# Optimization experiments

Hardware: AMD Instinct MI355X
Metric: run time of the kernel (lower is better)

The kernel has to match this reference:

```python
import jax, jax.numpy as jnp
import numpy as np

EMBED_DIM = 1024
HEAD_SIZE = 64
B, T = 8, 2048


def setup_inputs() -> dict:
    key = jax.random.key(0)
    kx, kk, kq, kv = jax.random.split(key, 4)
    s = EMBED_DIM ** -0.5  # linear init scale (arbitrary for baseline)
    return {
        "x": jax.random.normal(kx, (B, T, EMBED_DIM), dtype=jnp.float32),
        "Wk": jax.random.normal(kk, (EMBED_DIM, HEAD_SIZE), dtype=jnp.float32) * s,
        "Wq": jax.random.normal(kq, (EMBED_DIM, HEAD_SIZE), dtype=jnp.float32) * s,
        "Wv": jax.random.normal(kv, (EMBED_DIM, HEAD_SIZE), dtype=jnp.float32) * s,
    }


def reference(x, Wk, Wq, Wv):
    # x: [B, T, C]; projections: [C, H]
    k = jnp.einsum("btc,ch->bth", x, Wk)
    q = jnp.einsum("btc,ch->bth", x, Wq)
    v = jnp.einsum("btc,ch->bth", x, Wv)
    Tlen = x.shape[1]
    scores = jnp.einsum("bqh,bkh->bqk", q, k) * (Wk.shape[1] ** -0.5)  # [B,T,T]
    causal = jnp.tril(jnp.ones((Tlen, Tlen), dtype=bool))
    scores = jnp.where(causal, scores, -jnp.inf)
    weights = jax.nn.softmax(scores, axis=-1)  # dropout=0 (eval mode)
    return jnp.einsum("bqk,bkh->bqh", weights, v)
```

## Files before the change

### kernel.cpp

```cpp
#include <hip/hip_runtime.h>
#include <hip/hip_bf16.h>


typedef __attribute__((ext_vector_type(8))) __bf16 bf16x8;
typedef __attribute__((ext_vector_type(4))) float f32x4;

#define BT   16384
#define TLEN 2048
#define NB   8

__device__ __forceinline__ ushort f2bf(float f) {
    unsigned u = __builtin_bit_cast(unsigned, f);
    unsigned r = (u + 0x7FFFu + ((u >> 16) & 1u)) >> 16;
    return (ushort)r;
}

__global__ void wtrans_kernel(const float* __restrict__ Wk, const float* __restrict__ Wq,
                              const float* __restrict__ Wv, ushort* __restrict__ wtb) {
    int n = blockIdx.x;
    const float* W = (n < 64) ? Wk : (n < 128) ? Wq : Wv;
    float sc = (n >= 64 && n < 128) ? 0.125f : 1.0f;
    int h = n & 63;
    for (int k = threadIdx.x; k < 1024; k += 256)
        wtb[n * 1024 + k] = f2bf(W[(size_t)k * 64 + h] * sc);
}

__global__ __launch_bounds__(512, 3) void qkv_kernel2(
    const float* __restrict__ x, const ushort* __restrict__ wtb, ushort* __restrict__ kqv)
{
    __shared__ __align__(16) float ls_red[4][12][64][4];

    const int tid  = threadIdx.x;
    const int lane = tid & 63;
    const int wv   = tid >> 6;
    const int r    = wv & 1;
    const int h    = wv >> 1;
    const int m    = lane & 15;
    const int g    = lane >> 4;
    const int R0   = blockIdx.x * 32;
    const int arow = R0 + r * 16 + m;

    f32x4 acc[12];
    #pragma unroll
    for (int nt = 0; nt < 12; ++nt) acc[nt] = (f32x4){0.f, 0.f, 0.f, 0.f};

    const float*  xp = &x[(size_t)arow * 1024 + h * 256 + g * 8];
    const ushort* wb = &wtb[h * 256 + g * 8 + (size_t)m * 1024];

    #pragma unroll
    for (int st = 0; st < 8; ++st) {
        float4 a0 = *reinterpret_cast<const float4*>(xp);
        float4 a1 = *reinterpret_cast<const float4*>(xp + 4);
        xp += 32;
        union { ushort u[8]; bf16x8 v; } av;
        av.u[0] = f2bf(a0.x); av.u[1] = f2bf(a0.y); av.u[2] = f2bf(a0.z); av.u[3] = f2bf(a0.w);
        av.u[4] = f2bf(a1.x); av.u[5] = f2bf(a1.y); av.u[6] = f2bf(a1.z); av.u[7] = f2bf(a1.w);
        #pragma unroll
        for (int nt = 0; nt < 12; ++nt) {
            bf16x8 b = *reinterpret_cast<const bf16x8*>(wb + (size_t)nt * 16 * 1024 + st * 32);
            acc[nt] = __builtin_amdgcn_mfma_f32_16x16x32_bf16(av.v, b, acc[nt], 0, 0, 0);
        }
    }

    if (h & 1) {
        int slot = (h >> 1) * 2 + r;
        #pragma unroll
        for (int nt = 0; nt < 12; ++nt)
            *reinterpret_cast<f32x4*>(&ls_red[slot][nt][lane][0]) = acc[nt];
    }
    __syncthreads();
    if (!(h & 1)) {
        int slot = h + r;
        #pragma unroll
        for (int nt = 0; nt < 12; ++nt)
            acc[nt] += *reinterpret_cast<const f32x4*>(&ls_red[slot][nt][lane][0]);
    }
    __syncthreads();
    if (h == 2) {
        #pragma unroll
        for (int nt = 0; nt < 12; ++nt)
            *reinterpret_cast<f32x4*>(&ls_red[r][nt][lane][0]) = acc[nt];
    }
    __syncthreads();
    if (h == 0) {
        #pragma unroll
        for (int nt = 0; nt < 12; ++nt) {
            acc[nt] += *reinterpret_cast<const f32x4*>(&ls_red[r][nt][lane][0]);
            int s = nt >> 2;
            int c = (nt & 3) * 16 + m;
            #pragma unroll
            for (int j = 0; j < 4; ++j) {
                size_t row = (size_t)R0 + r * 16 + g * 4 + j;
                kqv[((size_t)s * BT + row) * 64 + c] = f2bf(acc[nt][j]);
            }
        }
    }
}

__global__ __launch_bounds__(512) void attn_kernel2(
    const ushort* __restrict__ qs, const ushort* __restrict__ ks,
    const ushort* __restrict__ vs, float* __restrict__ out)
{
    __shared__ __align__(16) ushort kt[2][64][72];
    __shared__ __align__(16) ushort vt[2][64][72];
    __shared__ __align__(16) ushort pl[8][16][72];

    const int bid = blockIdx.x;
    const int wg  = (bid & 7) * 32 + (bid >> 3);
    const int qt  = wg & 31;
    const int b   = wg >> 5;

    const int tid  = threadIdx.x;
    const int lane = tid & 63;
    const int wv   = tid >> 6;
    const int wq   = wv & 3;
    const int hf   = wv >> 2;
    const int m    = lane & 15;
    const int g    = lane >> 4;
    const int ko   = g * 8;
    const int rowb = g * 4;
    const size_t base = (size_t)b * TLEN;

    bf16x8 qa[2];
    {
        size_t row_g = base + (size_t)qt * 64 + wq * 16 + m;
        qa[0] = *reinterpret_cast<const bf16x8*>(&qs[row_g * 64 + 0 + ko]);
        qa[1] = *reinterpret_cast<const bf16x8*>(&qs[row_g * 64 + 32 + ko]);
    }

    f32x4 o[4];
    #pragma unroll
    for (int nt = 0; nt < 4; ++nt) o[nt] = (f32x4){0.f, 0.f, 0.f, 0.f};
    float mrun[4] = {-1e30f, -1e30f, -1e30f, -1e30f};
    float lrun[4] = {0.f, 0.f, 0.f, 0.f};

    const int hs   = tid >> 8;
    const int seg  = (tid & 255) & 3;
    const int srow = (tid & 255) >> 2;

    const int nit = (qt >> 1) + 1;
    for (int it = 0; it < nit; ++it) {
        int ts = 2 * it + hs;
        if (ts <= qt) {
            const ushort* ksrc = &ks[(base + (size_t)ts * 64 + srow) * 64 + seg * 16];
            *reinterpret_cast<uint4*>(&kt[hs][srow][seg * 16 + 0]) = *reinterpret_cast<const uint4*>(ksrc);
            *reinterpret_cast<uint4*>(&kt[hs][srow][seg * 16 + 8]) = *reinterpret_cast<const uint4*>(ksrc + 8);
            const ushort* vsrc = &vs[(base + (size_t)ts * 64 + srow) * 64 + seg * 16];
            union { uint4 v[2]; ushort u[16]; } tv;
            tv.v[0] = *reinterpret_cast<const uint4*>(vsrc);
            tv.v[1] = *reinterpret_cast<const uint4*>(vsrc + 8);
            #pragma unroll
            for (int i = 0; i < 16; ++i) vt[hs][seg * 16 + i][srow] = tv.u[i];
        }
        __syncthreads();

        int t = 2 * it + hf;
        if (t <= qt) {
            f32x4 s[4];
            #pragma unroll
            for (int nt = 0; nt < 4; ++nt) s[nt] = (f32x4){0.f, 0.f, 0.f, 0.f};
            #pragma unroll
            for (int kk = 0; kk < 2; ++kk) {
                #pragma unroll
                for (int nt = 0; nt < 4; ++nt) {
                    bf16x8 bb = *reinterpret_cast<const bf16x8*>(&kt[hf][nt * 16 + m][kk * 32 + ko]);
                    s[nt] = __builtin_amdgcn_mfma_f32_16x16x32_bf16(qa[kk], bb, s[nt], 0, 0, 0);
                }
            }
            if (t == qt) {
                #pragma unroll
                for (int nt = 0; nt < 4; ++nt)
                    #pragma unroll
                    for (int j = 0; j < 4; ++j)
                        if (nt * 16 + m > wq * 16 + rowb + j) s[nt][j] = -1e30f;
            }
            #pragma unroll
            for (int j = 0; j < 4; ++j) {
                float mx = fmaxf(fmaxf(s[0][j], s[1][j]), fmaxf(s[2][j], s[3][j]));
                #pragma unroll
                for (int d = 1; d < 16; d <<= 1) mx = fmaxf(mx, __shfl_xor(mx, d, 64));
                float mnew = fmaxf(mrun[j], mx);
                float corr = __expf(mrun[j] - mnew);
                mrun[j] = mnew;
                float p0 = __expf(s[0][j] - mnew);
                float p1 = __expf(s[1][j] - mnew);
                float p2 = __expf(s[2][j] - mnew);
                float p3 = __expf(s[3][j] - mnew);
                float ps = p0 + p1 + p2 + p3;
                #pragma unroll
                for (int d = 1; d < 16; d <<= 1) ps += __shfl_xor(ps, d, 64);
                lrun[j] = lrun[j] * corr + ps;
                #pragma unroll
                for (int nt = 0; nt < 4; ++nt) o[nt][j] *= corr;
                pl[wv][rowb + j][0 * 16 + m] = f2bf(p0);
                pl[wv][rowb + j][1 * 16 + m] = f2bf(p1);
                pl[wv][rowb + j][2 * 16 + m] = f2bf(p2);
                pl[wv][rowb + j][3 * 16 + m] = f2bf(p3);
            }
            asm volatile("s_waitcnt lgkmcnt(0)" ::: "memory");
            __builtin_amdgcn_sched_barrier(0);
            #pragma unroll
            for (int kk = 0; kk < 2; ++kk) {
                bf16x8 pa = *reinterpret_cast<const bf16x8*>(&pl[wv][m][kk * 32 + ko]);
                #pragma unroll
                for (int nt = 0; nt < 4; ++nt) {
                    bf16x8 vb = *reinterpret_cast<const bf16x8*>(&vt[hf][nt * 16 + m][kk * 32 + ko]);
                    o[nt] = __builtin_amdgcn_mfma_f32_16x16x32_bf16(pa, vb, o[nt], 0, 0, 0);
                }
            }
        }
        __syncthreads();
    }

    float* mg = reinterpret_cast<float*>(&kt[0][0][0]);
    float* st = reinterpret_cast<float*>(&vt[0][0][0]);
    if (hf == 1) {
        #pragma unroll
        for (int nt = 0; nt < 4; ++nt)
            *reinterpret_cast<f32x4*>(&mg[((wq * 4 + nt) * 64 + lane) * 4]) = o[nt];
        if (m == 0) {
            #pragma unroll
            for (int j = 0; j < 4; ++j) {
                st[(wq * 16 + rowb + j) * 2 + 0] = mrun[j];
                st[(wq * 16 + rowb + j) * 2 + 1] = lrun[j];
            }
        }
    }
    __syncthreads();
    if (hf == 0) {
        float ea[4], eb[4], li[4];
        #pragma unroll
        for (int j = 0; j < 4; ++j) {
            float m1 = st[(wq * 16 + rowb + j) * 2 + 0];
            float l1 = st[(wq * 16 + rowb + j) * 2 + 1];
            float mm = fmaxf(mrun[j], m1);
            ea[j] = __expf(mrun[j] - mm);
            eb[j] = __expf(m1 - mm);
            li[j] = 1.0f / (lrun[j] * ea[j] + l1 * eb[j]);
        }
        #pragma unroll
        for (int nt = 0; nt < 4; ++nt) {
            f32x4 ob = *reinterpret_cast<const f32x4*>(&mg[((wq * 4 + nt) * 64 + lane) * 4]);
            #pragma unroll
            for (int j = 0; j < 4; ++j) {
                size_t rrow = base + (size_t)qt * 64 + wq * 16 + rowb + j;
                out[rrow * 64 + nt * 16 + m] = (o[nt][j] * ea[j] + ob[j] * eb[j]) * li[j];
            }
        }
    }
}

extern "C" void kernel_launch(void* const* d_in, const int* in_sizes, int n_in,
                              void* d_out, int out_size, void* d_ws, size_t ws_size,
                              hipStream_t stream) {
    const float* x  = (const float*)d_in[0];
    const float* Wk = (const float*)d_in[1];
    const float* Wq = (const float*)d_in[2];
    const float* Wv = (const float*)d_in[3];
    float* out = (float*)d_out;

    ushort* ws   = (ushort*)d_ws;
    ushort* kqv  = ws;
    ushort* kbuf = ws;
    ushort* qbuf = ws + (size_t)BT * 64;
    ushort* vbuf = ws + (size_t)2 * BT * 64;
    ushort* wtb  = ws + (size_t)3 * BT * 64;

    wtrans_kernel<<<dim3(192), 256, 0, stream>>>(Wk, Wq, Wv, wtb);
    qkv_kernel2<<<dim3(512), 512, 0, stream>>>(x, wtb, kqv);
    attn_kernel2<<<dim3(256), 512, 0, stream>>>(qbuf, kbuf, vbuf, out);
}
```

Baseline: 186.6 us.

## Restructure QKV projection: each wave computes two row tiles, prefetch x, coalesced weight transpose

The QKV projection kernel now uses 256 threads per block, and each wave computes both 16-row tiles. Each weight fragment loaded is reused for two MFMAs, which halves weight loads per FLOP. Loads of x for the next k-step are prefetched into registers, and the cross-wave reduction is simplified. The weight transpose kernel now reads float4 coalesced rows, and f2bf uses the HIP intrinsic. The cost is twice the accumulator registers per wave (24 f32x4) and fewer waves per block, which may lower occupancy.

```diff
diff --git a/kernel.cpp b/kernel.cpp
--- a/kernel.cpp
+++ b/kernel.cpp
@@ -10,88 +10,103 @@
 #define NB   8
 
 __device__ __forceinline__ ushort f2bf(float f) {
-    unsigned u = __builtin_bit_cast(unsigned, f);
-    unsigned r = (u + 0x7FFFu + ((u >> 16) & 1u)) >> 16;
-    return (ushort)r;
+    __hip_bfloat16 h = __float2bfloat16(f);
+    return __builtin_bit_cast(ushort, h);
 }
 
 __global__ void wtrans_kernel(const float* __restrict__ Wk, const float* __restrict__ Wq,
                               const float* __restrict__ Wv, ushort* __restrict__ wtb) {
-    int n = blockIdx.x;
-    const float* W = (n < 64) ? Wk : (n < 128) ? Wq : Wv;
-    float sc = (n >= 64 && n < 128) ? 0.125f : 1.0f;
-    int h = n & 63;
-    for (int k = threadIdx.x; k < 1024; k += 256)
-        wtb[n * 1024 + k] = f2bf(W[(size_t)k * 64 + h] * sc);
-}
-
-__global__ __launch_bounds__(512, 3) void qkv_kernel2(
+    int idx = blockIdx.x * 256 + threadIdx.x;
+    int e   = idx * 4;
+    int s   = e >> 16;
+    int rem = e & 65535;
+    int k   = rem >> 6;
+    int h   = rem & 63;
+    const float* W = (s == 0) ? Wk : (s == 1) ? Wq : Wv;
+    float sc = (s == 1) ? 0.125f : 1.0f;
+    float4 v = *reinterpret_cast<const float4*>(&W[(size_t)k * 64 + h]);
+    wtb[(size_t)(s * 64 + h + 0) * 1024 + k] = f2bf(v.x * sc);
+    wtb[(size_t)(s * 64 + h + 1) * 1024 + k] = f2bf(v.y * sc);
+    wtb[(size_t)(s * 64 + h + 2) * 1024 + k] = f2bf(v.z * sc);
+    wtb[(size_t)(s * 64 + h + 3) * 1024 + k] = f2bf(v.w * sc);
+}
+
+__global__ __launch_bounds__(256, 2) void qkv_kernel3(
     const float* __restrict__ x, const ushort* __restrict__ wtb, ushort* __restrict__ kqv)
 {
-    __shared__ __align__(16) float ls_red[4][12][64][4];
+    __shared__ __align__(16) f32x4 red[2][24][64];
 
     const int tid  = threadIdx.x;
     const int lane = tid & 63;
-    const int wv   = tid >> 6;
-    const int r    = wv & 1;
-    const int h    = wv >> 1;
+    const int h    = tid >> 6;
     const int m    = lane & 15;
     const int g    = lane >> 4;
     const int R0   = blockIdx.x * 32;
-    const int arow = R0 + r * 16 + m;
-
-    f32x4 acc[12];
+
+    f32x4 acc[24];
     #pragma unroll
-    for (int nt = 0; nt < 12; ++nt) acc[nt] = (f32x4){0.f, 0.f, 0.f, 0.f};
-
-    const float*  xp = &x[(size_t)arow * 1024 + h * 256 + g * 8];
-    const ushort* wb = &wtb[h * 256 + g * 8 + (size_t)m * 1024];
+    for (int i = 0; i < 24; ++i) acc[i] = (f32x4){0.f, 0.f, 0.f, 0.f};
+
+    const float*  xp0 = &x[(size_t)(R0 + m)      * 1024 + h * 256 + g * 8];
+    const float*  xp1 = &x[(size_t)(R0 + 16 + m) * 1024 + h * 256 + g * 8];
+    const ushort* wb  = &wtb[(size_t)m * 1024 + h * 256 + g * 8];
+
+    float4 xa0a = *reinterpret_cast<const float4*>(xp0);
+    float4 xa0b = *reinterpret_cast<const float4*>(xp0 + 4);
+    float4 xa1a = *reinterpret_cast<const float4*>(xp1);
+    float4 xa1b = *reinterpret_cast<const float4*>(xp1 + 4);
 
     #pragma unroll
     for (int st = 0; st < 8; ++st) {
-        float4 a0 = *reinterpret_cast<const float4*>(xp);
-        float4 a1 = *reinterpret_cast<const float4*>(xp + 4);
-        xp += 32;
-        union { ushort u[8]; bf16x8 v; } av;
-        av.u[0] = f2bf(a0.x); av.u[1] = f2bf(a0.y); av.u[2] = f2bf(a0.z); av.u[3] = f2bf(a0.w);
-        av.u[4] = f2bf(a1.x); av.u[5] = f2bf(a1.y); av.u[6] = f2bf(a1.z); av.u[7] = f2bf(a1.w);
+        float4 xn0a, xn0b, xn1a, xn1b;
+        if (st < 7) {
+            xn0a = *reinterpret_cast<const float4*>(xp0 + (st + 1) * 32);
+            xn0b = *reinterpret_cast<const float4*>(xp0 + (st + 1) * 32 + 4);
+            xn1a = *reinterpret_cast<const float4*>(xp1 + (st + 1) * 32);
+            xn1b = *reinterpret_cast<const float4*>(xp1 + (st + 1) * 32 + 4);
+        }
+        union { ushort u[8]; bf16x8 v; } a0, a1;
+        a0.u[0] = f2bf(xa0a.x); a0.u[1] = f2bf(xa0a.y); a0.u[2] = f2bf(xa0a.z); a0.u[3] = f2bf(xa0a.w);
+        a0.u[4] = f2bf(xa0b.x); a0.u[5] = f2bf(xa0b.y); a0.u[6] = f2bf(xa0b.z); a0.u[7] = f2bf(xa0b.w);
+        a1.u[0] = f2bf(xa1a.x); a1.u[1] = f2bf(xa1a.y); a1.u[2] = f2bf(xa1a.z); a1.u[3] = f2bf(xa1a.w);
+        a1.u[4] = f2bf(xa1b.x); a1.u[5] = f2bf(xa1b.y); a1.u[6] = f2bf(xa1b.z); a1.u[7] = f2bf(xa1b.w);
         #pragma unroll
         for (int nt = 0; nt < 12; ++nt) {
             bf16x8 b = *reinterpret_cast<const bf16x8*>(wb + (size_t)nt * 16 * 1024 + st * 32);
-            acc[nt] = __builtin_amdgcn_mfma_f32_16x16x32_bf16(av.v, b, acc[nt], 0, 0, 0);
-        }
-    }
-
-    if (h & 1) {
-        int slot = (h >> 1) * 2 + r;
-        #pragma unroll
-        for (int nt = 0; nt < 12; ++nt)
-            *reinterpret_cast<f32x4*>(&ls_red[slot][nt][lane][0]) = acc[nt];
-    }
-    __syncthreads();
-    if (!(h & 1)) {
-        int slot = h + r;
-        #pragma unroll
-        for (int nt = 0; nt < 12; ++nt)
-            acc[nt] += *reinterpret_cast<const f32x4*>(&ls_red[slot][nt][lane][0]);
+            acc[nt]      = __builtin_amdgcn_mfma_f32_16x16x32_bf16(a0.v, b, acc[nt],      0, 0, 0);
+            acc[12 + nt] = __builtin_amdgcn_mfma_f32_16x16x32_bf16(a1.v, b, acc[12 + nt], 0, 0, 0);
+        }
+        xa0a = xn0a; xa0b = xn0b; xa1a = xn1a; xa1b = xn1b;
+    }
+
+    if (h == 1 || h == 3) {
+        #pragma unroll
+        for (int i = 0; i < 24; ++i) red[h >> 1][i][lane] = acc[i];
+    }
+    __syncthreads();
+    if (h == 0 || h == 2) {
+        #pragma unroll
+        for (int i = 0; i < 24; ++i) acc[i] += red[h >> 1][i][lane];
     }
     __syncthreads();
     if (h == 2) {
         #pragma unroll
-        for (int nt = 0; nt < 12; ++nt)
-            *reinterpret_cast<f32x4*>(&ls_red[r][nt][lane][0]) = acc[nt];
+        for (int i = 0; i < 24; ++i) red[0][i][lane] = acc[i];
     }
     __syncthreads();
     if (h == 0) {
         #pragma unroll
-        for (int nt = 0; nt < 12; ++nt) {
-            acc[nt] += *reinterpret_cast<const f32x4*>(&ls_red[r][nt][lane][0]);
-            int s = nt >> 2;
-            int c = (nt & 3) * 16 + m;
-            #pragma unroll
-            for (int j = 0; j < 4; ++j) {
-                size_t row = (size_t)R0 + r * 16 + g * 4 + j;
-                kqv[((size_t)s * BT + row) * 64 + c] = f2bf(acc[nt][j]);
+        for (int f = 0; f < 2; ++f) {
+            #pragma unroll
+            for (int nt = 0; nt < 12; ++nt) {
+                f32x4 a = acc[f * 12 + nt] + red[0][f * 12 + nt][lane];
+                int s = nt >> 2;
+                int c = (nt & 3) * 16 + m;
+                #pragma unroll
+                for (int j = 0; j < 4; ++j) {
+                    size_t row = (size_t)R0 + f * 16 + g * 4 + j;
+                    kqv[((size_t)s * BT + row) * 64 + c] = f2bf(a[j]);
+                }
             }
         }
     }
@@ -267,6 +282,6 @@
     ushort* wtb  = ws + (size_t)3 * BT * 64;
 
     wtrans_kernel<<<dim3(192), 256, 0, stream>>>(Wk, Wq, Wv, wtb);
-    qkv_kernel2<<<dim3(512), 512, 0, stream>>>(x, wtb, kqv);
+    qkv_kernel3<<<dim3(512), 256, 0, stream>>>(x, wtb, kqv);
     attn_kernel2<<<dim3(256), 512, 0, stream>>>(qbuf, kbuf, vbuf, out);
 }
```

After: 167.2 us. 10.4% less time.
